# Performance work log

Measured on AMD Instinct MI355X. Metric: run time of the kernel, lower is better.

## Reference

```python
import jax, jax.numpy as jnp
import numpy as np

C0 = 32        # num_feat_maps[0]
LD = 6         # latent_dim
NC = 1         # num_classes
B, P = 1, 96


def setup_inputs() -> dict:
    key = jax.random.key(0)
    ks = jax.random.split(key, 10)
    s = lambda fan_in: 1.0 / np.sqrt(fan_in)
    return {
        "feature_map": jax.random.normal(ks[0], (B, C0, P, P, P), dtype=jnp.float32),
        "z": jax.random.normal(ks[1], (B, LD), dtype=jnp.float32),
        "w1": jax.random.normal(ks[2], (C0, C0 + LD), dtype=jnp.float32) * s(C0 + LD),
        "b1": jnp.zeros((C0,), dtype=jnp.float32),
        "w2": jax.random.normal(ks[3], (C0, C0), dtype=jnp.float32) * s(C0),
        "b2": jnp.zeros((C0,), dtype=jnp.float32),
        "w3": jax.random.normal(ks[4], (C0, C0), dtype=jnp.float32) * s(C0),
        "b3": jnp.zeros((C0,), dtype=jnp.float32),
        "wl": jax.random.normal(ks[5], (NC, C0), dtype=jnp.float32) * s(C0),
        "bl": jnp.zeros((NC,), dtype=jnp.float32),
    }


def _pw(x, w, b):
    # 1x1x1 conv3d == pointwise channel GEMM: [B,Ci,X,Y,Z] x [Co,Ci] -> [B,Co,X,Y,Z]
    return jnp.einsum('bcxyz,oc->boxyz', x, w) + b[None, :, None, None, None]


def reference(feature_map, z, w1, b1, w2, b2, w3, b3, wl, bl):
    b, _, x_, y_, z_ = feature_map.shape
    # tile() on the unsqueezed z is equivalent to broadcasting over spatial dims
    zb = jnp.broadcast_to(z[:, :, None, None, None], (b, z.shape[1], x_, y_, z_))
    h = jnp.concatenate([feature_map, zb], axis=1)          # [B, C0+LD, P,P,P]
    h = jax.nn.relu(_pw(h, w1, b1))
    h = jax.nn.relu(_pw(h, w2, b2))
    h = jax.nn.relu(_pw(h, w3, b3))
    return _pw(h, wl, bl)                                    # [B, NC, P,P,P]
```

## Files before the change

### kernel.cpp

```cpp
#include <hip/hip_runtime.h>


typedef float    f32x16 __attribute__((ext_vector_type(16)));
typedef short    bf16x8 __attribute__((ext_vector_type(8)));
typedef unsigned u32x4  __attribute__((ext_vector_type(4)));

constexpr int NPTS  = 96 * 96 * 96;
constexpr int BLOCK = 256;
constexpr int GPW   = 4;
constexpr int NBLK  = NPTS / (32 * GPW * (BLOCK / 64));

__device__ __forceinline__ unsigned cvtpk(float lo, float hi) {
    unsigned d;
    asm("v_cvt_pk_bf16_f32 %0, %1, %2" : "=v"(d) : "v"(lo), "v"(hi));
    return d;
}
__device__ __forceinline__ float unlo(unsigned d) { return __uint_as_float(d << 16); }

__device__ __forceinline__ bf16x8 mk4(unsigned a, unsigned b, unsigned c, unsigned d) {
    u32x4 u; u.x = a; u.y = b; u.z = c; u.w = d;
    return __builtin_bit_cast(bf16x8, u);
}

__device__ __forceinline__ void swap32(unsigned a, unsigned b, unsigned& x, unsigned& y) {
    auto r = __builtin_amdgcn_permlane32_swap(a, b, false, false);
    x = r[0]; y = r[1];
}

__device__ __forceinline__ void load_wsplit(const float* __restrict__ W, int stride,
                                            int row, int koff, bf16x8& Hf, bf16x8& Lf) {
    const float2* p2 = reinterpret_cast<const float2*>(W + row * stride + koff);
    float2 q0 = p2[0], q1 = p2[1], q2 = p2[2], q3 = p2[3];
    unsigned h0 = cvtpk(q0.x, q0.y), h1 = cvtpk(q1.x, q1.y);
    unsigned h2 = cvtpk(q2.x, q2.y), h3 = cvtpk(q3.x, q3.y);
    unsigned l0 = cvtpk(q0.x - unlo(h0), q0.y - __uint_as_float(h0 & 0xffff0000u));
    unsigned l1 = cvtpk(q1.x - unlo(h1), q1.y - __uint_as_float(h1 & 0xffff0000u));
    unsigned l2 = cvtpk(q2.x - unlo(h2), q2.y - __uint_as_float(h2 & 0xffff0000u));
    unsigned l3 = cvtpk(q3.x - unlo(h3), q3.y - __uint_as_float(h3 & 0xffff0000u));
    Hf = mk4(h0, h1, h2, h3);
    Lf = mk4(l0, l1, l2, l3);
}

__device__ __forceinline__ void pack_frags(const f32x16 acc, bf16x8& F0, bf16x8& F1) {
    unsigned p0 = cvtpk(fmaxf(acc[0],  0.f), fmaxf(acc[1],  0.f));
    unsigned p1 = cvtpk(fmaxf(acc[2],  0.f), fmaxf(acc[3],  0.f));
    unsigned p2 = cvtpk(fmaxf(acc[4],  0.f), fmaxf(acc[5],  0.f));
    unsigned p3 = cvtpk(fmaxf(acc[6],  0.f), fmaxf(acc[7],  0.f));
    unsigned p4 = cvtpk(fmaxf(acc[8],  0.f), fmaxf(acc[9],  0.f));
    unsigned p5 = cvtpk(fmaxf(acc[10], 0.f), fmaxf(acc[11], 0.f));
    unsigned p6 = cvtpk(fmaxf(acc[12], 0.f), fmaxf(acc[13], 0.f));
    unsigned p7 = cvtpk(fmaxf(acc[14], 0.f), fmaxf(acc[15], 0.f));
    unsigned a0, a1, b0, b1, c0, c1, d0, d1;
    swap32(p0, p2, a0, a1); swap32(p1, p3, b0, b1);
    swap32(p4, p6, c0, c1); swap32(p5, p7, d0, d1);
    F0 = mk4(a0, b0, a1, b1);
    F1 = mk4(c0, d0, c1, d1);
}

__device__ __forceinline__ unsigned bias_word(float b) {
    float bhi = unlo(cvtpk(b, b));
    return cvtpk(b, b - bhi);
}

#define WLAYER(acc, WH0, WL0, WH1, WL1, F0, F1)                                   \
    acc = __builtin_amdgcn_mfma_f32_32x32x16_bf16(WH0, F0, acc, 0, 0, 0);         \
    acc = __builtin_amdgcn_mfma_f32_32x32x16_bf16(WL0, F0, acc, 0, 0, 0);         \
    acc = __builtin_amdgcn_mfma_f32_32x32x16_bf16(WH1, F1, acc, 0, 0, 0);         \
    acc = __builtin_amdgcn_mfma_f32_32x32x16_bf16(WL1, F1, acc, 0, 0, 0);

#define LOADG(arr, pt)                                                            \
    _Pragma("unroll")                                                             \
    for (int i = 0; i < 8; ++i) {                                                 \
        arr[i]     = fm[(koff + i) * NPTS + (pt)];                                \
        arr[8 + i] = fm[(16 + koff + i) * NPTS + (pt)];                           \
    }

#define COMPUTE(arr, pt)                                                          \
    {                                                                             \
        bf16x8 F0 = mk4(cvtpk(arr[0],  arr[1]),  cvtpk(arr[2],  arr[3]),          \
                        cvtpk(arr[4],  arr[5]),  cvtpk(arr[6],  arr[7]));         \
        bf16x8 F1 = mk4(cvtpk(arr[8],  arr[9]),  cvtpk(arr[10], arr[11]),         \
                        cvtpk(arr[12], arr[13]), cvtpk(arr[14], arr[15]));        \
        f32x16 acc = __builtin_amdgcn_mfma_f32_32x32x16_bf16(Ab1, Bone, zacc, 0, 0, 0); \
        WLAYER(acc, W1h0, W1l0, W1h1, W1l1, F0, F1)                               \
        pack_frags(acc, F0, F1);                                                  \
        acc = __builtin_amdgcn_mfma_f32_32x32x16_bf16(Ab2, Bone, zacc, 0, 0, 0);  \
        WLAYER(acc, W2h0, W2l0, W2h1, W2l1, F0, F1)                               \
        pack_frags(acc, F0, F1);                                                  \
        acc = __builtin_amdgcn_mfma_f32_32x32x16_bf16(Ab3, Bone, zacc, 0, 0, 0);  \
        WLAYER(acc, W3h0, W3l0, W3h1, W3l1, F0, F1)                               \
        float s = 0.f;                                                            \
        _Pragma("unroll")                                                         \
        for (int r = 0; r < 16; ++r) s = fmaf(wlr[r], fmaxf(acc[r], 0.f), s);     \
        unsigned px, py;                                                          \
        swap32(__float_as_uint(s), __float_as_uint(s), px, py);                   \
        float tot = __uint_as_float(px) + __uint_as_float(py) + blv;              \
        if (lane < 32) out[pt] = tot;                                             \
    }

__global__ __launch_bounds__(BLOCK, 3)
void fused_mlp_mfma(const float* __restrict__ fm, const float* __restrict__ z,
                    const float* __restrict__ w1, const float* __restrict__ b1,
                    const float* __restrict__ w2, const float* __restrict__ b2,
                    const float* __restrict__ w3, const float* __restrict__ b3,
                    const float* __restrict__ wl, const float* __restrict__ bl,
                    float* __restrict__ out)
{
    const int lane = threadIdx.x & 63;
    const int wid  = blockIdx.x * (BLOCK / 64) + (threadIdx.x >> 6);
    const int hl   = lane >> 5;
    const int col  = lane & 31;
    const int koff = 8 * hl;

    const int p0 = (wid * GPW + 0) * 32 + col;
    const int p1 = (wid * GPW + 1) * 32 + col;
    const int p2 = (wid * GPW + 2) * 32 + col;
    const int p3 = (wid * GPW + 3) * 32 + col;

    float va[16], vb[16];
    LOADG(va, p0)
    LOADG(vb, p1)

    bf16x8 W1h0, W1l0, W1h1, W1l1, W2h0, W2l0, W2h1, W2l1, W3h0, W3l0, W3h1, W3l1;
    load_wsplit(w1, 38, col, 0  + koff, W1h0, W1l0);
    load_wsplit(w1, 38, col, 16 + koff, W1h1, W1l1);
    load_wsplit(w2, 32, col, 0  + koff, W2h0, W2l0);
    load_wsplit(w2, 32, col, 16 + koff, W2h1, W2l1);
    load_wsplit(w3, 32, col, 0  + koff, W3h0, W3l0);
    load_wsplit(w3, 32, col, 16 + koff, W3h1, W3l1);

    float b1e = b1[col];
    b1e = fmaf(w1[col * 38 + 32], z[0], b1e);
    b1e = fmaf(w1[col * 38 + 33], z[1], b1e);
    b1e = fmaf(w1[col * 38 + 34], z[2], b1e);
    b1e = fmaf(w1[col * 38 + 35], z[3], b1e);
    b1e = fmaf(w1[col * 38 + 36], z[4], b1e);
    b1e = fmaf(w1[col * 38 + 37], z[5], b1e);
    const unsigned zero = 0u;
    bf16x8 Ab1  = mk4(hl ? zero : bias_word(b1e),     zero, zero, zero);
    bf16x8 Ab2  = mk4(hl ? zero : bias_word(b2[col]), zero, zero, zero);
    bf16x8 Ab3  = mk4(hl ? zero : bias_word(b3[col]), zero, zero, zero);
    bf16x8 Bone = mk4(hl ? zero : 0x3F803F80u,        zero, zero, zero);

    f32x16 wlr;
    #pragma unroll
    for (int r = 0; r < 16; ++r) wlr[r] = wl[(r & 3) + 8 * (r >> 2) + 4 * hl];
    const float blv = bl[0];

    f32x16 zacc;
    #pragma unroll
    for (int r = 0; r < 16; ++r) zacc[r] = 0.f;

    float vc[16];
    LOADG(vc, p2)
    COMPUTE(va, p0)

    float vd[16];
    LOADG(vd, p3)
    COMPUTE(vb, p1)

    COMPUTE(vc, p2)
    COMPUTE(vd, p3)
}

extern "C" void kernel_launch(void* const* d_in, const int* in_sizes, int n_in,
                              void* d_out, int out_size, void* d_ws, size_t ws_size,
                              hipStream_t stream)
{
    const float* fm = (const float*)d_in[0];
    const float* z  = (const float*)d_in[1];
    const float* w1 = (const float*)d_in[2];
    const float* b1 = (const float*)d_in[3];
    const float* w2 = (const float*)d_in[4];
    const float* b2 = (const float*)d_in[5];
    const float* w3 = (const float*)d_in[6];
    const float* b3 = (const float*)d_in[7];
    const float* wl = (const float*)d_in[8];
    const float* bl = (const float*)d_in[9];
    float* out = (float*)d_out;

    fused_mlp_mfma<<<NBLK, BLOCK, 0, stream>>>(
        fm, z, w1, b1, w2, b2, w3, b3, wl, bl, out);
}
```

Baseline: 185.2 us.

## Pre-pack feature map to bf16 pairs in a separate cast kernel

Adds a cast_pack kernel that converts the fp32 feature map into packed bf16 channel pairs in workspace, and has the main MLP kernel read the packed words instead of converting them itself. The main kernel then reads half the bytes, but the extra pass still reads the full fp32 input once and writes a half-size copy, so total HBM traffic goes up. It also adds a second kernel launch and relies on the workspace being large enough.

New measurement: 208.9 us. +12.8%, slower.

```diff
diff --git a/kernel.cpp b/kernel.cpp
--- a/kernel.cpp
+++ b/kernel.cpp
@@ -6,9 +6,11 @@
 typedef unsigned u32x4  __attribute__((ext_vector_type(4)));
 
 constexpr int NPTS  = 96 * 96 * 96;
+constexpr int NP4   = NPTS / 4;
 constexpr int BLOCK = 256;
 constexpr int GPW   = 4;
 constexpr int NBLK  = NPTS / (32 * GPW * (BLOCK / 64));
+constexpr int CASTB = 2048;
 
 __device__ __forceinline__ unsigned cvtpk(float lo, float hi) {
     unsigned d;
@@ -68,19 +70,38 @@
     acc = __builtin_amdgcn_mfma_f32_32x32x16_bf16(WH1, F1, acc, 0, 0, 0);         \
     acc = __builtin_amdgcn_mfma_f32_32x32x16_bf16(WL1, F1, acc, 0, 0, 0);
 
+__global__ __launch_bounds__(256)
+void cast_pack(const float* __restrict__ fm, unsigned* __restrict__ fmbp)
+{
+    const int stride = CASTB * 256;
+    const float4* __restrict__ f4 = reinterpret_cast<const float4*>(fm);
+    uint4* __restrict__ o4        = reinterpret_cast<uint4*>(fmbp);
+    const int total = 16 * NP4;
+    for (int i = blockIdx.x * 256 + threadIdx.x; i < total; i += stride) {
+        const int c2 = i / NP4;
+        const int j  = i - c2 * NP4;
+        float4 A = f4[(2 * c2)     * NP4 + j];
+        float4 B = f4[(2 * c2 + 1) * NP4 + j];
+        uint4 r;
+        r.x = cvtpk(A.x, B.x);
+        r.y = cvtpk(A.y, B.y);
+        r.z = cvtpk(A.z, B.z);
+        r.w = cvtpk(A.w, B.w);
+        o4[i] = r;
+    }
+}
+
 #define LOADG(arr, pt)                                                            \
     _Pragma("unroll")                                                             \
-    for (int i = 0; i < 8; ++i) {                                                 \
-        arr[i]     = fm[(koff + i) * NPTS + (pt)];                                \
-        arr[8 + i] = fm[(16 + koff + i) * NPTS + (pt)];                           \
+    for (int i = 0; i < 4; ++i) {                                                 \
+        arr[i]     = fmbp[(4 * hl + i) * NPTS + (pt)];                            \
+        arr[4 + i] = fmbp[(8 + 4 * hl + i) * NPTS + (pt)];                        \
     }
 
 #define COMPUTE(arr, pt)                                                          \
     {                                                                             \
-        bf16x8 F0 = mk4(cvtpk(arr[0],  arr[1]),  cvtpk(arr[2],  arr[3]),          \
-                        cvtpk(arr[4],  arr[5]),  cvtpk(arr[6],  arr[7]));         \
-        bf16x8 F1 = mk4(cvtpk(arr[8],  arr[9]),  cvtpk(arr[10], arr[11]),         \
-                        cvtpk(arr[12], arr[13]), cvtpk(arr[14], arr[15]));        \
+        bf16x8 F0 = mk4(arr[0], arr[1], arr[2], arr[3]);                          \
+        bf16x8 F1 = mk4(arr[4], arr[5], arr[6], arr[7]);                          \
         f32x16 acc = __builtin_amdgcn_mfma_f32_32x32x16_bf16(Ab1, Bone, zacc, 0, 0, 0); \
         WLAYER(acc, W1h0, W1l0, W1h1, W1l1, F0, F1)                               \
         pack_frags(acc, F0, F1);                                                  \
@@ -99,7 +120,7 @@
     }
 
 __global__ __launch_bounds__(BLOCK, 3)
-void fused_mlp_mfma(const float* __restrict__ fm, const float* __restrict__ z,
+void fused_mlp_mfma(const unsigned* __restrict__ fmbp, const float* __restrict__ z,
                     const float* __restrict__ w1, const float* __restrict__ b1,
                     const float* __restrict__ w2, const float* __restrict__ b2,
                     const float* __restrict__ w3, const float* __restrict__ b3,
@@ -117,7 +138,7 @@
     const int p2 = (wid * GPW + 2) * 32 + col;
     const int p3 = (wid * GPW + 3) * 32 + col;
 
-    float va[16], vb[16];
+    unsigned va[8], vb[8];
     LOADG(va, p0)
     LOADG(vb, p1)
 
@@ -151,11 +172,11 @@
     #pragma unroll
     for (int r = 0; r < 16; ++r) zacc[r] = 0.f;
 
-    float vc[16];
+    unsigned vc[8];
     LOADG(vc, p2)
     COMPUTE(va, p0)
 
-    float vd[16];
+    unsigned vd[8];
     LOADG(vd, p3)
     COMPUTE(vb, p1)
 
@@ -178,7 +199,9 @@
     const float* wl = (const float*)d_in[8];
     const float* bl = (const float*)d_in[9];
     float* out = (float*)d_out;
-
+    unsigned* fmbp = (unsigned*)d_ws;
+
+    cast_pack<<<CASTB, 256, 0, stream>>>(fm, fmbp);
     fused_mlp_mfma<<<NBLK, BLOCK, 0, stream>>>(
-        fm, z, w1, b1, w2, b2, w3, b3, wl, bl, out);
-}
+        fmbp, z, w1, b1, w2, b2, w3, b3, wl, bl, out);
+}
```
